# Performance work log

Hardware: AMD Instinct MI355X
Metric: run time of the kernel (lower is better)

The kernel has to match this reference:

```python
import jax, jax.numpy as jnp
import numpy as np
from itertools import permutations

# Static problem sizes: L=5 qubits, q=2**(L+1)=64 features, |G|=5!=120, 20 actions
L = 5
Q = 2 ** (L + 1)          # 64
G = 120                   # 5!
HID = 128
NACT = 20
B, T = 32, 64


def _build_tables():
    perms = list(permutations(range(L)))
    pidx = {p: i for i, p in enumerate(perms)}
    # inverse_table[i] = index of p_i^{-1}
    inv = [pidx[tuple(np.argsort(p))] for p in perms]
    # cayley[i, j] = index of p_i * p_j  (perm_prod(pi,pj) = tuple(pi[k] for k in pj))
    cayley = np.array([[pidx[tuple(pi[k] for k in pj)] for pj in perms] for pi in perms])
    # Hm[u, g] = index of permutation u * g^{-1} applied to x for group term g
    Hm = cayley[:, inv]
    # Gmap[u, p] = g such that Hm[u, g] == p  (row-wise bijection)
    Gmap = np.empty_like(Hm)
    Gmap[np.arange(G)[:, None], Hm] = np.arange(G)[None, :]
    # feature-level index maps: x_permuted = x[..., featperm[p]] matches torch
    # reshape(b,t,2,..,2).permute(0,1,2, g+3).reshape
    base = np.arange(Q).reshape((2,) * (L + 1))
    featperm = np.stack([
        base.transpose((0,) + tuple(i + 1 for i in p)).reshape(-1) for p in perms
    ])
    # action cosets: action a=(q0,q1) collects all perms with (p[0],p[1])==a
    acts = list(permutations(range(L), 2))
    aidx = {a: i for i, a in enumerate(acts)}
    coset_id = np.array([aidx[(p[0], p[1])] for p in perms])
    coset_size = np.bincount(coset_id, minlength=len(acts)).astype(np.float32)
    return featperm, Gmap, coset_id, coset_size


FEATPERM, GMAP, COSET_ID, COSET_SIZE = _build_tables()


def setup_inputs() -> dict:
    key = jax.random.key(0)
    ks = jax.random.split(key, 7)
    s = (2.0 / HID) ** 0.5  # kaiming-ish scale
    return {
        "x": jax.random.normal(ks[0], (B, T, Q), jnp.float32),
        "eq_weight": jax.random.normal(ks[1], (G, Q, HID), jnp.float32) * s,
        "eq_bias": jax.random.uniform(ks[2], (G, HID), jnp.float32, -0.01, 0.01),
        "W1": jax.random.normal(ks[3], (HID, HID), jnp.float32) * s,
        "b1": jax.random.uniform(ks[4], (HID,), jnp.float32, -0.01, 0.01),
        "Wout": jax.random.normal(ks[5], (HID, NACT), jnp.float32) * s,
        "bout": jax.random.uniform(ks[6], (NACT,), jnp.float32, -0.01, 0.01),
    }


def reference(x, eq_weight, eq_bias, W1, b1, Wout, bout):
    featperm = jnp.asarray(FEATPERM)          # (G, Q) int
    gmap = jnp.asarray(GMAP)                  # (G, G) int
    coset_id = jnp.asarray(COSET_ID)          # (G,) int
    coset_size = jnp.asarray(COSET_SIZE)      # (NACT,) float

    # all qubit-level permutations of the input: (G, b, t, q)
    Xp = jnp.moveaxis(x[..., featperm], 2, 0)
    # Equivariant layer for ALL u at once:
    # result(u) = (1/G) * sum_p Xp[p] @ W[Gmap[u,p]] + mean_g bias[g]
    Wu = eq_weight[gmap]                      # (G_u, G_p, Q, HID)
    e = jnp.einsum('pbtq,upqh->ubth', Xp, Wu) / G + eq_bias.mean(0)
    h = jax.nn.relu(e)
    h = jax.nn.relu(h @ W1 + b1)              # second hidden layer (dropout_rate=0)
    out = h @ Wout + bout                     # (G, b, t, NACT)
    m = out.mean(-1)                          # (G, b, t)
    # y_i = mean over u in coset_i of m[u]
    y = jax.ops.segment_sum(m, coset_id, num_segments=NACT)
    y = y / coset_size[:, None, None]
    return jnp.transpose(y, (1, 2, 0))        # (b, t, NACT)
```

## Files before the change

kernel.cpp:

```cpp
#include <hip/hip_runtime.h>

typedef _Float16 f16;
typedef __attribute__((ext_vector_type(8))) _Float16 f16x8;
typedef __attribute__((ext_vector_type(4))) float f32x4;
typedef __attribute__((ext_vector_type(4))) unsigned int u32x4;
typedef __attribute__((ext_vector_type(8))) unsigned short ushort8;

#define QF   64
#define GG   120
#define HID  128
#define NACT 20
#define BTOT 2048

#define WEFF_OFF 0u
#define XH_OFF   1966080u
#define W1F_OFF  2490368u
#define MISC_OFF 2523136u
#define ABUF_OFF 2524224u

template <typename T>
__device__ __forceinline__ void keepv(T& v) { asm volatile("" : "+v"(v)); }

__device__ __forceinline__ unsigned idx_to_packed(int i) {
    unsigned avail = 0x43210u, pp = 0u;
    const int fct[4] = {24, 6, 2, 1};
#pragma unroll
    for (int k = 0; k < 4; ++k) {
        int d = i / fct[k]; i -= d * fct[k];
        pp |= ((avail >> (4 * d)) & 0xFu) << (4 * k);
        unsigned mask = (1u << (4 * d)) - 1u;
        avail = (avail & mask) | ((avail >> 4) & ~mask);
    }
    pp |= (avail & 0xFu) << 16;
    return pp;
}

__device__ __forceinline__ int packed_to_idx(unsigned pp) {
    const int fct[4] = {24, 6, 2, 1};
    int idx = 0;
#pragma unroll
    for (int k = 0; k < 4; ++k) {
        unsigned pk = (pp >> (4 * k)) & 0xFu;
        int c = 0;
#pragma unroll
        for (int j = k + 1; j < 5; ++j)
            c += (int)(((pp >> (4 * j)) & 0xFu) < pk);
        idx += c * fct[k];
    }
    return idx;
}

__device__ __forceinline__ unsigned compose_packed(unsigned pa, unsigned pb) {
    unsigned pc = 0;
#pragma unroll
    for (int k = 0; k < 5; ++k) {
        unsigned bk = (pb >> (4 * k)) & 0xFu;
        pc |= ((pa >> (4 * bk)) & 0xFu) << (4 * k);
    }
    return pc;
}

__device__ __forceinline__ unsigned invert_packed(unsigned pp) {
    unsigned pi = 0;
#pragma unroll
    for (int k = 0; k < 5; ++k)
        pi |= (unsigned)k << (4 * ((pp >> (4 * k)) & 0xFu));
    return pi;
}

__device__ __forceinline__ unsigned s4_packed(int i) {
    unsigned avail = 0x3210u, pp = 0u;
    const int f3[3] = {6, 2, 1};
#pragma unroll
    for (int k = 0; k < 3; ++k) {
        int d = i / f3[k]; i -= d * f3[k];
        pp |= ((avail >> (4 * d)) & 0xFu) << (4 * k);
        unsigned mask = (1u << (4 * d)) - 1u;
        avail = (avail & mask) | ((avail >> 4) & ~mask);
    }
    pp |= (avail & 0xFu) << 12;
    pp |= 4u << 16;
    return pp;
}

__device__ __forceinline__ unsigned crep_pp(int t) {
    unsigned pp = 0x43210u;
    pp &= ~(0xFu << (4 * t));
    pp &= ~(0xFu << 16);
    pp |= 4u << (4 * t);
    pp |= (unsigned)t << 16;
    return pp;
}

__device__ __forceinline__ int bitperm_r(unsigned ppi, int r) {
    int val = r & 32;
#pragma unroll
    for (int k = 0; k < 5; ++k) {
        int pik = (ppi >> (4 * k)) & 0xF;
        val |= ((r >> (4 - pik)) & 1) << (4 - k);
    }
    return val;
}

__device__ __forceinline__ int coset_member(int a, int e) {
    int i = a >> 2, jj = a & 3;
    int j = jj + (jj >= i ? 1 : 0);
    unsigned mask = 0x1Fu & ~(1u << i) & ~(1u << j);
    int d0 = __builtin_ctz(mask); mask &= mask - 1u;
    int d1 = __builtin_ctz(mask); mask &= mask - 1u;
    int d2 = __builtin_ctz(mask);
    int k0 = e >> 1;
    int p2 = k0 == 0 ? d0 : (k0 == 1 ? d1 : d2);
    int r0 = k0 == 0 ? d1 : d0;
    int r1 = k0 == 2 ? d1 : d2;
    int p3 = (e & 1) ? r1 : r0;
    int p4 = (e & 1) ? r0 : r1;
    unsigned pp = (unsigned)i | ((unsigned)j << 4) | ((unsigned)p2 << 8)
                | ((unsigned)p3 << 12) | ((unsigned)p4 << 16);
    return packed_to_idx(pp);
}

__device__ __forceinline__ unsigned short f2h(float f) {
    f16 h = (f16)f;
    return __builtin_bit_cast(unsigned short, h);
}
__device__ __forceinline__ unsigned pk2(float a, float b) {
    return (unsigned)f2h(a) | ((unsigned)f2h(b) << 16);
}

__global__ void prep_stage1(const float* __restrict__ x, const float* __restrict__ W1,
                            const float* __restrict__ eq_bias, const float* __restrict__ Wout,
                            const float* __restrict__ bout, const float* __restrict__ eqw,
                            float* __restrict__ misc,
                            unsigned short* __restrict__ xh,
                            unsigned short* __restrict__ w1f, float* __restrict__ Acan) {
    __shared__ int sg[24];
    __shared__ int sq[24][8];
    int b = blockIdx.x, t = threadIdx.x;
    if (b < 40) {
        int c = b >> 3, rbase = (b & 7) * 8;
        if (t < 24) sg[t] = packed_to_idx(compose_packed(s4_packed(t), crep_pp(c)));
        if (t < 192) {
            int si = t >> 3;
            sq[si][t & 7] = bitperm_r(invert_packed(s4_packed(si)), rbase + (t & 7));
        }
        __syncthreads();
        int h4 = (t & 31) * 4, rslot = t >> 5;
        f32x4 acc = {0.f, 0.f, 0.f, 0.f};
#pragma unroll
        for (int si = 0; si < 24; ++si) {
            f32x4 v = *(const f32x4*)(eqw + (unsigned)(sg[si] * QF + sq[si][rslot]) * HID + h4);
            acc = acc + v;
        }
        *(f32x4*)(Acan + (unsigned)(c * QF + rbase + rslot) * HID + h4) = acc;
    } else if (b < 552) {
        int idx = (b - 40) * 256 + t;
        xh[idx] = f2h(x[idx]);
    } else if (b < 560) {
        int idx = (b - 552) * 256 + t;
        int fg = idx >> 6, lane = idx & 63;
        int nt = fg >> 2, ks = fg & 3;
        int n = nt * 16 + (lane & 15), kg = lane >> 4;
        ushort8 v;
#pragma unroll
        for (int j = 0; j < 8; ++j) {
            int h = ks * 32 + ((j >> 2) << 4) + (kg << 2) + (j & 3);
            v[j] = f2h(W1[h * HID + n]);
        }
        *(ushort8*)(w1f + idx * 8) = v;
    } else {
        if (t < HID) {
            float s = 0.f;
            for (int g = 0; g < GG; ++g) s += eq_bias[g * HID + t];
            misc[t] = s * (1.f / GG);
            float wv = 0.f;
            for (int n = 0; n < NACT; ++n) wv += Wout[t * NACT + n];
            misc[HID + t] = wv * (1.f / NACT);
            if (t == 0) {
                float c = 0.f;
                for (int n = 0; n < NACT; ++n) c += bout[n];
                misc[2 * HID] = c * (1.f / NACT);
            }
        }
    }
}

__global__ void weff_stage2(const float* __restrict__ Acan,
                            unsigned short* __restrict__ weff) {
    __shared__ float Wacc[HID][QF + 1];
    __shared__ int rp[5][64];
    int u = blockIdx.x, t = threadIdx.x;
    unsigned upk = idx_to_packed(u);
    for (int i = t; i < 5 * 64; i += 256)
        rp[i >> 6][i & 63] = bitperm_r(compose_packed(upk, crep_pp(i >> 6)), i & 63);
    __syncthreads();
    int h = t & 127, qg = t >> 7;
    for (int i = 0; i < 32; ++i) {
        int q = qg * 32 + i;
        float s = 0.f;
#pragma unroll
        for (int c = 0; c < 5; ++c)
            s += Acan[(unsigned)(c * QF + rp[c][q]) * HID + h];
        Wacc[h][q] = s * (1.f / GG);
    }
    __syncthreads();
    for (int e = t; e < 1024; e += 256) {
        int fg = e >> 6, lane = e & 63;
        int hm = fg >> 1, ks = fg & 1;
        int hh = hm * 16 + (lane & 15), q0 = ks * 32 + (lane >> 4) * 8;
        ushort8 v;
#pragma unroll
        for (int j = 0; j < 8; ++j) v[j] = f2h(Wacc[hh][q0 + j]);
        *(ushort8*)(weff + (unsigned)(u * 16 + fg) * 64 * 8 + lane * 8) = v;
    }
}

__device__ __forceinline__ f32x4 mfma16(f16x8 a, f16x8 b, f32x4 c) {
    return __builtin_amdgcn_mfma_f32_16x16x32_f16(a, b, c, 0, 0, 0);
}

__global__ __launch_bounds__(128, 2)
void mlp_mfma(const unsigned short* __restrict__ xh,
              const unsigned short* __restrict__ weff,
              const unsigned short* __restrict__ w1f,
              const float* __restrict__ b1,
              const float* __restrict__ misc,
              float* __restrict__ out) {
    __shared__ __align__(16) unsigned short w1s[16384];
    __shared__ __align__(16) unsigned short wefs[8192];
    __shared__ float miscs[2 * HID];
    __shared__ float b1s[HID];

    int bid0 = blockIdx.x;
    int bid = (bid0 & 7) * 80 + (bid0 >> 3);
    int tile = bid & 31, a = bid >> 5;
    int rowbase = tile * 64;
    int t = threadIdx.x;
    int w = t >> 6, lane = t & 63;
    int lm = lane & 15, kg = lane >> 4;
    int xbase = rowbase + w * 32;

    int u0 = coset_member(a, 0);
#pragma unroll
    for (int i = 0; i < 16; ++i)
        *(u32x4*)(w1s + (i * 128 + t) * 8) = *(const u32x4*)(w1f + (i * 128 + t) * 8);
#pragma unroll
    for (int i = 0; i < 8; ++i)
        *(u32x4*)(wefs + (i * 128 + t) * 8) =
            *(const u32x4*)(weff + (unsigned)u0 * 8192 + (i * 128 + t) * 8);
    miscs[t] = misc[t];
    miscs[128 + t] = misc[128 + t];
    b1s[t] = b1[t];
    float cb = misc[2 * HID];

    f16x8 xb[2][2];
#pragma unroll
    for (int xt = 0; xt < 2; ++xt)
#pragma unroll
        for (int ks = 0; ks < 2; ++ks) {
            int off = (xbase + xt * 16 + lm) * QF + ks * 32 + kg * 8;
            xb[xt][ks] = *(const f16x8*)(xh + off);
            keepv(xb[xt][ks]);
        }
    __syncthreads();

    float macc[2][4];
#pragma unroll
    for (int xt = 0; xt < 2; ++xt)
#pragma unroll
        for (int r = 0; r < 4; ++r) macc[xt][r] = 0.f;

#pragma unroll 1
    for (int ui = 0; ui < 6; ++ui) {
        bool hasNext = (ui < 5);
        u32x4 pf[8];
        if (hasNext) {
            int un = coset_member(a, ui + 1);
            const unsigned short* wsrc = weff + (unsigned)un * 8192;
#pragma unroll
            for (int i = 0; i < 8; ++i)
                pf[i] = *(const u32x4*)(wsrc + (i * 128 + t) * 8);
        }

        f32x4 acc[2][8];
#pragma unroll
        for (int xt = 0; xt < 2; ++xt)
#pragma unroll
            for (int hm = 0; hm < 8; ++hm) acc[xt][hm] = (f32x4){0.f, 0.f, 0.f, 0.f};
#pragma unroll
        for (int hm = 0; hm < 8; ++hm)
#pragma unroll
            for (int ks = 0; ks < 2; ++ks) {
                f16x8 wf = *(const f16x8*)(wefs + ((hm * 2 + ks) * 64 + lane) * 8);
#pragma unroll
                for (int xt = 0; xt < 2; ++xt)
                    acc[xt][hm] = mfma16(wf, xb[xt][ks], acc[xt][hm]);
            }

        __syncthreads();
        if (hasNext) {
#pragma unroll
            for (int i = 0; i < 8; ++i)
                *(u32x4*)(wefs + (i * 128 + t) * 8) = pf[i];
        }

        f32x4 acc2[2][8];
#pragma unroll
        for (int xt = 0; xt < 2; ++xt)
#pragma unroll
            for (int nt = 0; nt < 8; ++nt) acc2[xt][nt] = (f32x4){0.f, 0.f, 0.f, 0.f};
#pragma unroll
        for (int ks = 0; ks < 4; ++ks) {
            f32x4 bm0 = *(const f32x4*)(miscs + (2 * ks) * 16 + kg * 4);
            f32x4 bm1 = *(const f32x4*)(miscs + (2 * ks + 1) * 16 + kg * 4);
            f16x8 pa[2];
#pragma unroll
            for (int xt = 0; xt < 2; ++xt) {
                f32x4 e0 = acc[xt][2 * ks] + bm0;
                f32x4 e1 = acc[xt][2 * ks + 1] + bm1;
#pragma unroll
                for (int r = 0; r < 4; ++r) {
                    e0[r] = e0[r] > 0.f ? e0[r] : 0.f;
                    e1[r] = e1[r] > 0.f ? e1[r] : 0.f;
                }
                u32x4 ph = {pk2(e0[0], e0[1]), pk2(e0[2], e0[3]),
                            pk2(e1[0], e1[1]), pk2(e1[2], e1[3])};
                pa[xt] = __builtin_bit_cast(f16x8, ph);
            }
#pragma unroll
            for (int nt = 0; nt < 8; ++nt) {
                f16x8 wf = *(const f16x8*)(w1s + ((nt * 4 + ks) * 64 + lane) * 8);
#pragma unroll
                for (int xt = 0; xt < 2; ++xt)
                    acc2[xt][nt] = mfma16(pa[xt], wf, acc2[xt][nt]);
            }
        }

#pragma unroll
        for (int nt = 0; nt < 8; ++nt) {
            float bb = b1s[nt * 16 + lm];
            float wm = miscs[HID + nt * 16 + lm];
#pragma unroll
            for (int xt = 0; xt < 2; ++xt)
#pragma unroll
                for (int r = 0; r < 4; ++r) {
                    float v = acc2[xt][nt][r] + bb;
                    v = v > 0.f ? v : 0.f;
                    macc[xt][r] += v * wm;
                }
        }
        __syncthreads();
    }

#pragma unroll
    for (int off = 1; off < 16; off <<= 1)
#pragma unroll
        for (int xt = 0; xt < 2; ++xt)
#pragma unroll
            for (int r = 0; r < 4; ++r)
                macc[xt][r] += __shfl_xor(macc[xt][r], off, 64);
    if (lm == 0) {
#pragma unroll
        for (int xt = 0; xt < 2; ++xt)
#pragma unroll
            for (int r = 0; r < 4; ++r)
                out[(unsigned)(xbase + xt * 16 + kg * 4 + r) * NACT + a] =
                    macc[xt][r] * (1.f / 6.f) + cb;
    }
}

extern "C" void kernel_launch(void* const* d_in, const int* in_sizes, int n_in,
                              void* d_out, int out_size, void* d_ws, size_t ws_size,
                              hipStream_t stream) {
    const float* x       = (const float*)d_in[0];
    const float* eqw     = (const float*)d_in[1];
    const float* eq_bias = (const float*)d_in[2];
    const float* W1      = (const float*)d_in[3];
    const float* b1      = (const float*)d_in[4];
    const float* Wout    = (const float*)d_in[5];
    const float* bout    = (const float*)d_in[6];
    float* out           = (float*)d_out;

    char* ws = (char*)d_ws;
    unsigned short* weff = (unsigned short*)(ws + WEFF_OFF);
    unsigned short* xhb  = (unsigned short*)(ws + XH_OFF);
    unsigned short* w1f  = (unsigned short*)(ws + W1F_OFF);
    float* misc   = (float*)(ws + MISC_OFF);
    float* Acan   = (float*)(ws + ABUF_OFF);

    hipLaunchKernelGGL(prep_stage1, dim3(561), dim3(256), 0, stream,
                       x, W1, eq_bias, Wout, bout, eqw, misc, xhb, w1f, Acan);
    hipLaunchKernelGGL(weff_stage2, dim3(120), dim3(256), 0, stream,
                       Acan, weff);
    hipLaunchKernelGGL(mlp_mfma, dim3(640), dim3(128), 0, stream,
                       xhb, weff, w1f, b1, misc, out);
}
```

Measured before the change: 41.36 us.

## Load per-coset effective weights directly into registers, drop LDS staging and barriers

The per-coset first-layer weight fragments no longer go through a shared-memory buffer. Each wave now loads them straight from global memory into 16 f16x8 registers, and the next coset's weights are fetched right after the first-layer MFMAs are issued. This removes two __syncthreads per iteration and the LDS round-trip. In exchange, register pressure rises noticeably (64 extra VGPRs under launch_bounds(128,2)), and each wave issues its own global loads of the same weights, so the two waves in a block both read them.

Result: slower. 116.5 us (+181.6%).

```diff
diff --git a/kernel.cpp b/kernel.cpp
--- a/kernel.cpp
+++ b/kernel.cpp
@@ -227,7 +227,6 @@
               const float* __restrict__ misc,
               float* __restrict__ out) {
     __shared__ __align__(16) unsigned short w1s[16384];
-    __shared__ __align__(16) unsigned short wefs[8192];
     __shared__ float miscs[2 * HID];
     __shared__ float b1s[HID];
 
@@ -240,14 +239,9 @@
     int lm = lane & 15, kg = lane >> 4;
     int xbase = rowbase + w * 32;
 
-    int u0 = coset_member(a, 0);
 #pragma unroll
     for (int i = 0; i < 16; ++i)
         *(u32x4*)(w1s + (i * 128 + t) * 8) = *(const u32x4*)(w1f + (i * 128 + t) * 8);
-#pragma unroll
-    for (int i = 0; i < 8; ++i)
-        *(u32x4*)(wefs + (i * 128 + t) * 8) =
-            *(const u32x4*)(weff + (unsigned)u0 * 8192 + (i * 128 + t) * 8);
     miscs[t] = misc[t];
     miscs[128 + t] = misc[128 + t];
     b1s[t] = b1[t];
@@ -264,6 +258,15 @@
         }
     __syncthreads();
 
+    f16x8 wf[16];
+    {
+        int u0 = coset_member(a, 0);
+        const unsigned short* wsrc = weff + (unsigned)u0 * 8192;
+#pragma unroll
+        for (int f = 0; f < 16; ++f)
+            wf[f] = *(const f16x8*)(wsrc + (f * 64 + lane) * 8);
+    }
+
     float macc[2][4];
 #pragma unroll
     for (int xt = 0; xt < 2; ++xt)
@@ -272,48 +275,32 @@
 
 #pragma unroll 1
     for (int ui = 0; ui < 6; ++ui) {
-        bool hasNext = (ui < 5);
-        u32x4 pf[8];
-        if (hasNext) {
+        f32x4 acc[2][8];
+#pragma unroll
+        for (int xt = 0; xt < 2; ++xt)
+#pragma unroll
+            for (int hm = 0; hm < 8; ++hm) acc[xt][hm] = (f32x4){0.f, 0.f, 0.f, 0.f};
+#pragma unroll
+        for (int hm = 0; hm < 8; ++hm)
+#pragma unroll
+            for (int ks = 0; ks < 2; ++ks)
+#pragma unroll
+                for (int xt = 0; xt < 2; ++xt)
+                    acc[xt][hm] = mfma16(wf[hm * 2 + ks], xb[xt][ks], acc[xt][hm]);
+
+        if (ui < 5) {
             int un = coset_member(a, ui + 1);
             const unsigned short* wsrc = weff + (unsigned)un * 8192;
 #pragma unroll
-            for (int i = 0; i < 8; ++i)
-                pf[i] = *(const u32x4*)(wsrc + (i * 128 + t) * 8);
-        }
-
-        f32x4 acc[2][8];
-#pragma unroll
-        for (int xt = 0; xt < 2; ++xt)
-#pragma unroll
-            for (int hm = 0; hm < 8; ++hm) acc[xt][hm] = (f32x4){0.f, 0.f, 0.f, 0.f};
-#pragma unroll
-        for (int hm = 0; hm < 8; ++hm)
-#pragma unroll
-            for (int ks = 0; ks < 2; ++ks) {
-                f16x8 wf = *(const f16x8*)(wefs + ((hm * 2 + ks) * 64 + lane) * 8);
-#pragma unroll
-                for (int xt = 0; xt < 2; ++xt)
-                    acc[xt][hm] = mfma16(wf, xb[xt][ks], acc[xt][hm]);
-            }
-
-        __syncthreads();
-        if (hasNext) {
-#pragma unroll
-            for (int i = 0; i < 8; ++i)
-                *(u32x4*)(wefs + (i * 128 + t) * 8) = pf[i];
-        }
-
-        f32x4 acc2[2][8];
-#pragma unroll
-        for (int xt = 0; xt < 2; ++xt)
-#pragma unroll
-            for (int nt = 0; nt < 8; ++nt) acc2[xt][nt] = (f32x4){0.f, 0.f, 0.f, 0.f};
+            for (int f = 0; f < 16; ++f)
+                wf[f] = *(const f16x8*)(wsrc + (f * 64 + lane) * 8);
+        }
+
+        f16x8 pa[2][4];
 #pragma unroll
         for (int ks = 0; ks < 4; ++ks) {
             f32x4 bm0 = *(const f32x4*)(miscs + (2 * ks) * 16 + kg * 4);
             f32x4 bm1 = *(const f32x4*)(miscs + (2 * ks + 1) * 16 + kg * 4);
-            f16x8 pa[2];
 #pragma unroll
             for (int xt = 0; xt < 2; ++xt) {
                 f32x4 e0 = acc[xt][2 * ks] + bm0;
@@ -325,16 +312,24 @@
                 }
                 u32x4 ph = {pk2(e0[0], e0[1]), pk2(e0[2], e0[3]),
                             pk2(e1[0], e1[1]), pk2(e1[2], e1[3])};
-                pa[xt] = __builtin_bit_cast(f16x8, ph);
+                pa[xt][ks] = __builtin_bit_cast(f16x8, ph);
             }
+        }
+
+        f32x4 acc2[2][8];
+#pragma unroll
+        for (int xt = 0; xt < 2; ++xt)
+#pragma unroll
+            for (int nt = 0; nt < 8; ++nt) acc2[xt][nt] = (f32x4){0.f, 0.f, 0.f, 0.f};
+#pragma unroll
+        for (int ks = 0; ks < 4; ++ks)
 #pragma unroll
             for (int nt = 0; nt < 8; ++nt) {
-                f16x8 wf = *(const f16x8*)(w1s + ((nt * 4 + ks) * 64 + lane) * 8);
+                f16x8 wb = *(const f16x8*)(w1s + ((nt * 4 + ks) * 64 + lane) * 8);
 #pragma unroll
                 for (int xt = 0; xt < 2; ++xt)
-                    acc2[xt][nt] = mfma16(pa[xt], wf, acc2[xt][nt]);
+                    acc2[xt][nt] = mfma16(pa[xt][ks], wb, acc2[xt][nt]);
             }
-        }
 
 #pragma unroll
         for (int nt = 0; nt < 8; ++nt) {
@@ -349,7 +344,6 @@
                     macc[xt][r] += v * wm;
                 }
         }
-        __syncthreads();
     }
 
 #pragma unroll
```

## Fuse x fp16 conversion into MLP kernel and rebalance prep kernels

Applied to the files above, without the earlier changes.

Removes the separate x-to-fp16 conversion pass and its workspace buffer. The MLP kernel now loads fp32 x directly and converts it to fp16 in registers. The W1 fragment packing and the bias/Wout reductions move out of the first prep kernel into the weff kernel, so the first kernel only computes the canonical sums. This cuts a global round trip for x and shrinks the first kernel's grid, at the cost of reading twice as many bytes of x inside the main kernel.

Result: no change. 41.96 us (+1.5%).

```diff
diff --git a/kernel.cpp b/kernel.cpp
--- a/kernel.cpp
+++ b/kernel.cpp
@@ -13,10 +13,9 @@
 #define BTOT 2048
 
 #define WEFF_OFF 0u
-#define XH_OFF   1966080u
-#define W1F_OFF  2490368u
-#define MISC_OFF 2523136u
-#define ABUF_OFF 2524224u
+#define W1F_OFF  1966080u
+#define MISC_OFF 1998848u
+#define ABUF_OFF 1999936u
 
 template <typename T>
 __device__ __forceinline__ void keepv(T& v) { asm volatile("" : "+v"(v)); }
@@ -128,36 +127,66 @@
     return (unsigned)f2h(a) | ((unsigned)f2h(b) << 16);
 }
 
-__global__ void prep_stage1(const float* __restrict__ x, const float* __restrict__ W1,
-                            const float* __restrict__ eq_bias, const float* __restrict__ Wout,
-                            const float* __restrict__ bout, const float* __restrict__ eqw,
-                            float* __restrict__ misc,
-                            unsigned short* __restrict__ xh,
-                            unsigned short* __restrict__ w1f, float* __restrict__ Acan) {
+__device__ __forceinline__ f32x4 mfma16(f16x8 a, f16x8 b, f32x4 c) {
+    return __builtin_amdgcn_mfma_f32_16x16x32_f16(a, b, c, 0, 0, 0);
+}
+
+__global__ void k1_acanon(const float* __restrict__ eqw, float* __restrict__ Acan) {
     __shared__ int sg[24];
     __shared__ int sq[24][8];
     int b = blockIdx.x, t = threadIdx.x;
-    if (b < 40) {
-        int c = b >> 3, rbase = (b & 7) * 8;
-        if (t < 24) sg[t] = packed_to_idx(compose_packed(s4_packed(t), crep_pp(c)));
-        if (t < 192) {
-            int si = t >> 3;
-            sq[si][t & 7] = bitperm_r(invert_packed(s4_packed(si)), rbase + (t & 7));
-        }
+    int c = b >> 3, rbase = (b & 7) * 8;
+    if (t < 24) sg[t] = packed_to_idx(compose_packed(s4_packed(t), crep_pp(c)));
+    if (t < 192) {
+        int si = t >> 3;
+        sq[si][t & 7] = bitperm_r(invert_packed(s4_packed(si)), rbase + (t & 7));
+    }
+    __syncthreads();
+    int h4 = (t & 31) * 4, rslot = t >> 5;
+    f32x4 acc = {0.f, 0.f, 0.f, 0.f};
+#pragma unroll
+    for (int si = 0; si < 24; ++si) {
+        f32x4 v = *(const f32x4*)(eqw + (unsigned)(sg[si] * QF + sq[si][rslot]) * HID + h4);
+        acc = acc + v;
+    }
+    *(f32x4*)(Acan + (unsigned)(c * QF + rbase + rslot) * HID + h4) = acc;
+}
+
+__global__ void k2_weff(const float* __restrict__ Acan, const float* __restrict__ W1,
+                        const float* __restrict__ eq_bias, const float* __restrict__ Wout,
+                        const float* __restrict__ bout,
+                        unsigned short* __restrict__ weff,
+                        unsigned short* __restrict__ w1f, float* __restrict__ misc) {
+    __shared__ float Wacc[HID][QF + 1];
+    __shared__ int rp[5][64];
+    int b = blockIdx.x, t = threadIdx.x;
+    if (b < 120) {
+        int u = b;
+        unsigned upk = idx_to_packed(u);
+        for (int i = t; i < 5 * 64; i += 256)
+            rp[i >> 6][i & 63] = bitperm_r(compose_packed(upk, crep_pp(i >> 6)), i & 63);
         __syncthreads();
-        int h4 = (t & 31) * 4, rslot = t >> 5;
-        f32x4 acc = {0.f, 0.f, 0.f, 0.f};
-#pragma unroll
-        for (int si = 0; si < 24; ++si) {
-            f32x4 v = *(const f32x4*)(eqw + (unsigned)(sg[si] * QF + sq[si][rslot]) * HID + h4);
-            acc = acc + v;
-        }
-        *(f32x4*)(Acan + (unsigned)(c * QF + rbase + rslot) * HID + h4) = acc;
-    } else if (b < 552) {
-        int idx = (b - 40) * 256 + t;
-        xh[idx] = f2h(x[idx]);
-    } else if (b < 560) {
-        int idx = (b - 552) * 256 + t;
+        int h = t & 127, qg = t >> 7;
+        for (int i = 0; i < 32; ++i) {
+            int q = qg * 32 + i;
+            float s = 0.f;
+#pragma unroll
+            for (int c = 0; c < 5; ++c)
+                s += Acan[(unsigned)(c * QF + rp[c][q]) * HID + h];
+            Wacc[h][q] = s * (1.f / GG);
+        }
+        __syncthreads();
+        for (int e = t; e < 1024; e += 256) {
+            int fg = e >> 6, lane = e & 63;
+            int hm = fg >> 1, ks = fg & 1;
+            int hh = hm * 16 + (lane & 15), q0 = ks * 32 + (lane >> 4) * 8;
+            ushort8 v;
+#pragma unroll
+            for (int j = 0; j < 8; ++j) v[j] = f2h(Wacc[hh][q0 + j]);
+            *(ushort8*)(weff + (unsigned)(u * 16 + fg) * 64 * 8 + lane * 8) = v;
+        }
+    } else if (b < 128) {
+        int idx = (b - 120) * 256 + t;
         int fg = idx >> 6, lane = idx & 63;
         int nt = fg >> 2, ks = fg & 3;
         int n = nt * 16 + (lane & 15), kg = lane >> 4;
@@ -185,42 +214,8 @@
     }
 }
 
-__global__ void weff_stage2(const float* __restrict__ Acan,
-                            unsigned short* __restrict__ weff) {
-    __shared__ float Wacc[HID][QF + 1];
-    __shared__ int rp[5][64];
-    int u = blockIdx.x, t = threadIdx.x;
-    unsigned upk = idx_to_packed(u);
-    for (int i = t; i < 5 * 64; i += 256)
-        rp[i >> 6][i & 63] = bitperm_r(compose_packed(upk, crep_pp(i >> 6)), i & 63);
-    __syncthreads();
-    int h = t & 127, qg = t >> 7;
-    for (int i = 0; i < 32; ++i) {
-        int q = qg * 32 + i;
-        float s = 0.f;
-#pragma unroll
-        for (int c = 0; c < 5; ++c)
-            s += Acan[(unsigned)(c * QF + rp[c][q]) * HID + h];
-        Wacc[h][q] = s * (1.f / GG);
-    }
-    __syncthreads();
-    for (int e = t; e < 1024; e += 256) {
-        int fg = e >> 6, lane = e & 63;
-        int hm = fg >> 1, ks = fg & 1;
-        int hh = hm * 16 + (lane & 15), q0 = ks * 32 + (lane >> 4) * 8;
-        ushort8 v;
-#pragma unroll
-        for (int j = 0; j < 8; ++j) v[j] = f2h(Wacc[hh][q0 + j]);
-        *(ushort8*)(weff + (unsigned)(u * 16 + fg) * 64 * 8 + lane * 8) = v;
-    }
-}
-
-__device__ __forceinline__ f32x4 mfma16(f16x8 a, f16x8 b, f32x4 c) {
-    return __builtin_amdgcn_mfma_f32_16x16x32_f16(a, b, c, 0, 0, 0);
-}
-
 __global__ __launch_bounds__(128, 2)
-void mlp_mfma(const unsigned short* __restrict__ xh,
+void mlp_mfma(const float* __restrict__ x,
               const unsigned short* __restrict__ weff,
               const unsigned short* __restrict__ w1f,
               const float* __restrict__ b1,
@@ -258,8 +253,13 @@
     for (int xt = 0; xt < 2; ++xt)
 #pragma unroll
         for (int ks = 0; ks < 2; ++ks) {
-            int off = (xbase + xt * 16 + lm) * QF + ks * 32 + kg * 8;
-            xb[xt][ks] = *(const f16x8*)(xh + off);
+            const float* xp = x + (unsigned)(xbase + xt * 16 + lm) * QF + ks * 32 + kg * 8;
+            f32x4 a0 = *(const f32x4*)xp;
+            f32x4 a1 = *(const f32x4*)(xp + 4);
+            ushort8 v;
+            v[0] = f2h(a0[0]); v[1] = f2h(a0[1]); v[2] = f2h(a0[2]); v[3] = f2h(a0[3]);
+            v[4] = f2h(a1[0]); v[5] = f2h(a1[1]); v[6] = f2h(a1[2]); v[7] = f2h(a1[3]);
+            xb[xt][ks] = __builtin_bit_cast(f16x8, v);
             keepv(xb[xt][ks]);
         }
     __syncthreads();
@@ -329,10 +329,10 @@
             }
 #pragma unroll
             for (int nt = 0; nt < 8; ++nt) {
-                f16x8 wf = *(const f16x8*)(w1s + ((nt * 4 + ks) * 64 + lane) * 8);
+                f16x8 wb = *(const f16x8*)(w1s + ((nt * 4 + ks) * 64 + lane) * 8);
 #pragma unroll
                 for (int xt = 0; xt < 2; ++xt)
-                    acc2[xt][nt] = mfma16(pa[xt], wf, acc2[xt][nt]);
+                    acc2[xt][nt] = mfma16(pa[xt], wb, acc2[xt][nt]);
             }
         }
 
@@ -383,15 +383,13 @@
 
     char* ws = (char*)d_ws;
     unsigned short* weff = (unsigned short*)(ws + WEFF_OFF);
-    unsigned short* xhb  = (unsigned short*)(ws + XH_OFF);
     unsigned short* w1f  = (unsigned short*)(ws + W1F_OFF);
     float* misc   = (float*)(ws + MISC_OFF);
     float* Acan   = (float*)(ws + ABUF_OFF);
 
-    hipLaunchKernelGGL(prep_stage1, dim3(561), dim3(256), 0, stream,
-                       x, W1, eq_bias, Wout, bout, eqw, misc, xhb, w1f, Acan);
-    hipLaunchKernelGGL(weff_stage2, dim3(120), dim3(256), 0, stream,
-                       Acan, weff);
+    hipLaunchKernelGGL(k1_acanon, dim3(40), dim3(256), 0, stream, eqw, Acan);
+    hipLaunchKernelGGL(k2_weff, dim3(129), dim3(256), 0, stream,
+                       Acan, W1, eq_bias, Wout, bout, weff, w1f, misc);
     hipLaunchKernelGGL(mlp_mfma, dim3(640), dim3(128), 0, stream,
-                       xhb, weff, w1f, b1, misc, out);
-}
+                       x, weff, w1f, b1, misc, out);
+}
```
